# Performance work log

Measured on AMD Instinct MI355X. Metric: run time of the kernel, lower is better.

## Reference

```python
import jax, jax.numpy as jnp
import numpy as np

B, E, H, N_TAYLOR = 8192, 256, 4096, 4
BN_EPS = 1e-5


def setup_inputs() -> dict:
    key = jax.random.key(0)
    ks = jax.random.split(key, 6)
    s = 0.02
    return {
        "z1": jax.random.normal(ks[0], (B, E), jnp.float32),
        "z2": jax.random.normal(ks[1], (B, E), jnp.float32),
        "p1": jax.random.normal(ks[2], (B, E), jnp.float32),
        "p2": jax.random.normal(ks[3], (B, E), jnp.float32),
        "W1": jax.random.normal(ks[4], (E, H), jnp.float32) * s,
        "gamma": jnp.ones((H,), jnp.float32),
        "beta": jnp.zeros((H,), jnp.float32),
        "W2": jax.random.normal(ks[5], (H, E), jnp.float32) * s,
        "b2": jnp.zeros((E,), jnp.float32),
        "lamda_inv": jnp.asarray(100.0, jnp.float32),
    }


def _predictor(z, W1, gamma, beta, W2, b2):
    h = z @ W1                                   # [B, H]
    mu = jnp.mean(h, axis=0)
    var = jnp.mean(jnp.square(h - mu), axis=0)   # biased var (torch BN training)
    h = (h - mu) * jax.lax.rsqrt(var + BN_EPS) * gamma + beta
    h = jax.nn.relu(h)
    return h @ W2 + b2                           # [B, E]


def _l2norm(x):
    n = jnp.linalg.norm(x, axis=1, keepdims=True)
    return x / jnp.maximum(n, 1e-12)


def _mec(view1, view2, lamda_inv):
    v1, v2 = _l2norm(view1), _l2norm(view2)
    c = (v1 @ v2.T) / lamda_inv                  # [B, B]
    power = c
    sum_p = jnp.zeros_like(c)
    for k in range(1, N_TAYLOR + 1):
        if k > 1:
            power = power @ c
        sign = 1.0 if (k + 1) % 2 == 0 else -1.0
        sum_p = sum_p + sign * power / k
    return jnp.trace(sum_p)


def reference(z1, z2, p1, p2, W1, gamma, beta, W2, b2, lamda_inv):
    q1 = _predictor(z1, W1, gamma, beta, W2, b2)
    q2 = _predictor(z2, W1, gamma, beta, W2, b2)
    loss = (_mec(p1, q2, lamda_inv) + _mec(p2, q1, lamda_inv)) * 0.5 / B
    return -loss * lamda_inv
```

## Files before the change

### kernel.cpp

```cpp
#include <hip/hip_runtime.h>

#define B_ROWS 8192
#define E_DIM  256
#define H_DIM  4096

typedef __attribute__((ext_vector_type(8))) short short8;
typedef __attribute__((ext_vector_type(4))) float f32x4;

typedef __attribute__((address_space(1))) const void* gas1_t;
typedef __attribute__((address_space(3))) void*       las3_t;

__device__ __forceinline__ float b2f(unsigned short s) {
    return __uint_as_float(((unsigned)s) << 16);
}
__device__ __forceinline__ unsigned short f2b(float f) {
    unsigned u = __float_as_uint(f);
    u += 0x7fffu + ((u >> 16) & 1u);
    return (unsigned short)(u >> 16);
}

__device__ __forceinline__ int swz(int row, int slot) {
    return slot ^ ((row >> 1) & 3);
}

__global__ void k_transpose_cast(const float* __restrict__ in,
                                 unsigned short* __restrict__ out,
                                 int R, int C) {
    __shared__ float tile[32][33];
    const int c0 = blockIdx.x * 32, r0 = blockIdx.y * 32;
    const int tx = threadIdx.x & 31, ty = threadIdx.x >> 5;
#pragma unroll
    for (int j = 0; j < 4; ++j)
        tile[ty * 4 + j][tx] = in[(size_t)(r0 + ty * 4 + j) * C + c0 + tx];
    __syncthreads();
#pragma unroll
    for (int j = 0; j < 4; ++j)
        out[(size_t)(c0 + ty * 4 + j) * R + r0 + tx] = f2b(tile[tx][ty * 4 + j]);
}

__global__ void k_cast_bf16(const float* __restrict__ in,
                            unsigned short* __restrict__ out, int n4) {
    int i = blockIdx.x * blockDim.x + threadIdx.x;
    if (i < n4) {
        float4 v = ((const float4*)in)[i];
        ushort4 o;
        o.x = f2b(v.x); o.y = f2b(v.y); o.z = f2b(v.z); o.w = f2b(v.w);
        ((ushort4*)out)[i] = o;
    }
}

__global__ __launch_bounds__(256) void k_gemm1(
    const unsigned short* __restrict__ A, const unsigned short* __restrict__ Bt,
    unsigned short* __restrict__ Cout,
    float* __restrict__ cs, float* __restrict__ cs2,
    int M, int N, int K) {
    constexpr int BK = 32, BM = 128, BN = 128;
    constexpr int MI = 4, NI = 4;
    __shared__ __align__(16) short As[BM * BK];
    __shared__ __align__(16) short Bs[BN * BK];

    const int t = threadIdx.x;
    const int lane = t & 63, wv = t >> 6;
    const int wr = wv >> 1, wc = wv & 1;
    const int l15 = lane & 15, quad = lane >> 4;
    const int m0 = blockIdx.y * BM, n0 = blockIdx.x * BN;

    f32x4 acc[MI][NI] = {};

    for (int k0 = 0; k0 < K; k0 += BK) {
#pragma unroll
        for (int q = 0; q < 2; ++q) {
            int u = q * 256 + t;
            int row = u >> 2, kc = swz(row, u & 3);
            const short* gp = (const short*)A + (size_t)(m0 + row) * K + k0 + kc * 8;
            short* lp = As + (size_t)(q * 256 + (wv << 6)) * 8;
            __builtin_amdgcn_global_load_lds((gas1_t)gp, (las3_t)lp, 16, 0, 0);
        }
#pragma unroll
        for (int q = 0; q < 2; ++q) {
            int u = q * 256 + t;
            int row = u >> 2, kc = swz(row, u & 3);
            const short* gp = (const short*)Bt + (size_t)(n0 + row) * K + k0 + kc * 8;
            short* lp = Bs + (size_t)(q * 256 + (wv << 6)) * 8;
            __builtin_amdgcn_global_load_lds((gas1_t)gp, (las3_t)lp, 16, 0, 0);
        }
        __syncthreads();

        short8 af[MI], bfr[NI];
#pragma unroll
        for (int mi = 0; mi < MI; ++mi) {
            int row = wr * 64 + mi * 16 + l15;
            af[mi] = *(const short8*)(As + row * BK + (swz(row, quad) << 3));
        }
#pragma unroll
        for (int ni = 0; ni < NI; ++ni) {
            int row = wc * 64 + ni * 16 + l15;
            bfr[ni] = *(const short8*)(Bs + row * BK + (swz(row, quad) << 3));
        }
#pragma unroll
        for (int mi = 0; mi < MI; ++mi)
#pragma unroll
            for (int ni = 0; ni < NI; ++ni)
                acc[mi][ni] = __builtin_amdgcn_mfma_f32_16x16x32_bf16(
                    af[mi], bfr[ni], acc[mi][ni], 0, 0, 0);
        __syncthreads();
    }

#pragma unroll
    for (int ni = 0; ni < NI; ++ni) {
        float s = 0.f, s2 = 0.f;
#pragma unroll
        for (int mi = 0; mi < MI; ++mi)
#pragma unroll
            for (int r = 0; r < 4; ++r) {
                int row = m0 + wr * 64 + mi * 16 + quad * 4 + r;
                int col = n0 + wc * 64 + ni * 16 + l15;
                float v = acc[mi][ni][r];
                Cout[(size_t)row * N + col] = f2b(v);
                s += v; s2 += v * v;
            }
        s  += __shfl_xor(s, 16);  s  += __shfl_xor(s, 32);
        s2 += __shfl_xor(s2, 16); s2 += __shfl_xor(s2, 32);
        if (quad == 0) {
            int col = n0 + wc * 64 + ni * 16 + l15;
            atomicAdd(&cs[col], s);
            atomicAdd(&cs2[col], s2);
        }
    }
}

__global__ void k_bnprep(const float* __restrict__ sum, const float* __restrict__ sumsq,
                         const float* __restrict__ gamma, const float* __restrict__ beta,
                         unsigned* __restrict__ ssb) {
    int j = blockIdx.x * 256 + threadIdx.x;
    float mu = sum[j] * (1.f / B_ROWS);
    float var = sumsq[j] * (1.f / B_ROWS) - mu * mu;
    float sc = gamma[j] * rsqrtf(var + 1e-5f);
    float sh = beta[j] - mu * sc;
    ssb[j] = ((unsigned)f2b(sc) << 16) | (unsigned)f2b(sh);
}

__device__ __forceinline__ short8 bnrelu8(uint4 hv, uint4 sa, uint4 sb) {
    const unsigned short* hu = (const unsigned short*)&hv;
    const unsigned* wa = (const unsigned*)&sa;
    const unsigned* wb = (const unsigned*)&sb;
    short8 o;
#pragma unroll
    for (int j = 0; j < 8; ++j) {
        unsigned w = j < 4 ? wa[j] : wb[j - 4];
        float sc = __uint_as_float(w & 0xffff0000u);
        float sh = __uint_as_float(w << 16);
        float v = fmaxf(b2f(hu[j]) * sc + sh, 0.f);
        o[j] = (short)f2b(v);
    }
    return o;
}

__global__ __launch_bounds__(256) void k_gemm2d(
    const unsigned short* __restrict__ A, const unsigned short* __restrict__ Bt,
    float* __restrict__ Cout, const float* __restrict__ bias,
    const unsigned* __restrict__ ssb,
    int M, int N, int K) {
    constexpr int BK = 32, BM = 64, BN = 128;
    constexpr int MI = 2, NI = 4;
    __shared__ __align__(16) short As[2][BM * BK];
    __shared__ __align__(16) short Bs[2][BN * BK];

    const int t = threadIdx.x;
    const int lane = t & 63, wv = t >> 6;
    const int wr = wv >> 1, wc = wv & 1;
    const int l15 = lane & 15, quad = lane >> 4;
    const int m0 = blockIdx.y * BM, n0 = blockIdx.x * BN;

    const int Kc = K / gridDim.z;
    const int kbeg = blockIdx.z * Kc;
    const int ITERS = Kc / BK;

    const int arow = t >> 2, akc = t & 3;
    const unsigned short* hp = A + (size_t)(m0 + arow) * K + akc * 8;
    const unsigned* ssp = ssb + akc * 8;
    const int awoff = arow * BK + (swz(arow, akc) << 3);

    const unsigned short* bp0 = Bt + (size_t)(n0 + arow) * K + akc * 8;
    const unsigned short* bp1 = Bt + (size_t)(n0 + 64 + arow) * K + akc * 8;
    const int bwoff0 = arow * BK + (swz(arow, akc) << 3);
    const int bwoff1 = (64 + arow) * BK + (swz(64 + arow, akc) << 3);

    f32x4 acc[MI][NI] = {};

    uint4 hreg = *(const uint4*)(hp + kbeg);
    uint4 sa = *(const uint4*)(ssp + kbeg);
    uint4 sb = *(const uint4*)(ssp + kbeg + 4);
    uint4 b0 = *(const uint4*)(bp0 + kbeg);
    uint4 b1 = *(const uint4*)(bp1 + kbeg);

    for (int i = 0; i < ITERS; ++i) {
        const int k0 = kbeg + i * BK;
        short* Ab = As[i & 1];
        short* Bb = Bs[i & 1];

        *(short8*)(Ab + awoff) = bnrelu8(hreg, sa, sb);
        *(uint4*)(Bb + bwoff0) = b0;
        *(uint4*)(Bb + bwoff1) = b1;
        __syncthreads();

        const int kn = (i + 1 < ITERS) ? k0 + BK : kbeg;
        hreg = *(const uint4*)(hp + kn);
        sa = *(const uint4*)(ssp + kn);
        sb = *(const uint4*)(ssp + kn + 4);
        b0 = *(const uint4*)(bp0 + kn);
        b1 = *(const uint4*)(bp1 + kn);

        short8 af[MI], bfr[NI];
#pragma unroll
        for (int mi = 0; mi < MI; ++mi) {
            int row = wr * 32 + mi * 16 + l15;
            af[mi] = *(const short8*)(Ab + row * BK + (swz(row, quad) << 3));
        }
#pragma unroll
        for (int ni = 0; ni < NI; ++ni) {
            int row = wc * 64 + ni * 16 + l15;
            bfr[ni] = *(const short8*)(Bb + row * BK + (swz(row, quad) << 3));
        }
#pragma unroll
        for (int mi = 0; mi < MI; ++mi)
#pragma unroll
            for (int ni = 0; ni < NI; ++ni)
                acc[mi][ni] = __builtin_amdgcn_mfma_f32_16x16x32_bf16(
                    af[mi], bfr[ni], acc[mi][ni], 0, 0, 0);
    }

#pragma unroll
    for (int mi = 0; mi < MI; ++mi)
#pragma unroll
        for (int ni = 0; ni < NI; ++ni)
#pragma unroll
            for (int r = 0; r < 4; ++r) {
                int row = m0 + wr * 32 + mi * 16 + quad * 4 + r;
                int col = n0 + wc * 64 + ni * 16 + l15;
                float v = acc[mi][ni][r];
                if (blockIdx.z == 0) v += bias[col];
                atomicAdd(&Cout[(size_t)row * N + col], v);
            }
}

__global__ __launch_bounds__(256) void k_ntc(
    const float* __restrict__ x0, const float* __restrict__ x1,
    const float* __restrict__ x2, const float* __restrict__ x3,
    unsigned short* __restrict__ o0, unsigned short* __restrict__ o1,
    unsigned short* __restrict__ o2, unsigned short* __restrict__ o3) {
    const int z = blockIdx.y;
    const float* x = z == 0 ? x0 : z == 1 ? x1 : z == 2 ? x2 : x3;
    unsigned short* out = z == 0 ? o0 : z == 1 ? o1 : z == 2 ? o2 : o3;

    __shared__ float tile[32][264];
    __shared__ float red[32][8];
    __shared__ float invs[32];
    const int t = threadIdx.x;
    const int r0 = blockIdx.x * 32;

#pragma unroll
    for (int i = 0; i < 8; ++i) {
        int u = i * 256 + t;
        int row = u >> 6, cp = (u & 63) * 4;
        float4 v = *(const float4*)(x + (size_t)(r0 + row) * E_DIM + cp);
        *(float4*)&tile[row][cp] = v;
    }
    __syncthreads();
    {
        int row = t >> 3, cg = (t & 7) * 32;
        float s = 0.f;
#pragma unroll
        for (int j = 0; j < 32; ++j) { float v = tile[row][cg + j]; s += v * v; }
        red[row][t & 7] = s;
    }
    __syncthreads();
    if (t < 32) {
        float s = 0.f;
#pragma unroll
        for (int j = 0; j < 8; ++j) s += red[t][j];
        invs[t] = 1.f / fmaxf(sqrtf(s), 1e-12f);
    }
    __syncthreads();
    {
        int row = t & 31, cb = (t >> 5) * 32;
        float inv = invs[row];
#pragma unroll
        for (int j = 0; j < 32; ++j) {
            int c = cb + j;
            out[(size_t)c * B_ROWS + r0 + row] = f2b(tile[row][c] * inv);
        }
    }
}

#define GKS 16
__global__ __launch_bounds__(256) void k_gram(
    const unsigned short* __restrict__ p1T, const unsigned short* __restrict__ q2T,
    const unsigned short* __restrict__ p2T, const unsigned short* __restrict__ q1T,
    float* __restrict__ Ma, float* __restrict__ Mb) {
    constexpr int BK = 32;
    const int mec = blockIdx.z >> 4, kz = blockIdx.z & 15;
    const unsigned short* A = mec ? p2T : p1T;
    const unsigned short* Bt = mec ? q1T : q2T;
    float* Mout = mec ? Mb : Ma;

    __shared__ __align__(16) short As[64 * BK];
    __shared__ __align__(16) short Bs[64 * BK];

    const int t = threadIdx.x;
    const int lane = t & 63, wv = t >> 6;
    const int wr = wv >> 1, wc = wv & 1;
    const int l15 = lane & 15, quad = lane >> 4;
    const int m0 = blockIdx.y * 64, n0 = blockIdx.x * 64;
    const int kbeg = kz * (B_ROWS / GKS);

    f32x4 acc[2][2] = {};

    for (int k0 = kbeg; k0 < kbeg + B_ROWS / GKS; k0 += BK) {
        {
            int row = t >> 2, kc = swz(row, t & 3);
            const short* gpa = (const short*)A + (size_t)(m0 + row) * B_ROWS + k0 + kc * 8;
            short* lpa = As + (size_t)(wv << 6) * 8;
            __builtin_amdgcn_global_load_lds((gas1_t)gpa, (las3_t)lpa, 16, 0, 0);
            const short* gpb = (const short*)Bt + (size_t)(n0 + row) * B_ROWS + k0 + kc * 8;
            short* lpb = Bs + (size_t)(wv << 6) * 8;
            __builtin_amdgcn_global_load_lds((gas1_t)gpb, (las3_t)lpb, 16, 0, 0);
        }
        __syncthreads();

        short8 af[2], bfr[2];
#pragma unroll
        for (int mi = 0; mi < 2; ++mi) {
            int row = wr * 32 + mi * 16 + l15;
            af[mi] = *(const short8*)(As + row * BK + (swz(row, quad) << 3));
        }
#pragma unroll
        for (int ni = 0; ni < 2; ++ni) {
            int row = wc * 32 + ni * 16 + l15;
            bfr[ni] = *(const short8*)(Bs + row * BK + (swz(row, quad) << 3));
        }
#pragma unroll
        for (int mi = 0; mi < 2; ++mi)
#pragma unroll
            for (int ni = 0; ni < 2; ++ni)
                acc[mi][ni] = __builtin_amdgcn_mfma_f32_16x16x32_bf16(
                    af[mi], bfr[ni], acc[mi][ni], 0, 0, 0);
        __syncthreads();
    }

#pragma unroll
    for (int mi = 0; mi < 2; ++mi)
#pragma unroll
        for (int ni = 0; ni < 2; ++ni)
#pragma unroll
            for (int r = 0; r < 4; ++r) {
                int row = m0 + wr * 32 + mi * 16 + quad * 4 + r;
                int col = n0 + wc * 32 + ni * 16 + l15;
                atomicAdd(&Mout[(size_t)row * E_DIM + col], acc[mi][ni][r]);
            }
}

__global__ void k_m2(const float* __restrict__ Ma, const float* __restrict__ Mb,
                     float* __restrict__ M2a, float* __restrict__ M2b) {
    const float* M = blockIdx.z ? Mb : Ma;
    float* M2 = blockIdx.z ? M2b : M2a;
    int b = blockIdx.x * 16 + (threadIdx.x & 15);
    int a = blockIdx.y * 16 + (threadIdx.x >> 4);
    float s = 0.f;
    for (int k = 0; k < E_DIM; ++k) s += M[a * E_DIM + k] * M[k * E_DIM + b];
    M2[a * E_DIM + b] = s;
}

__global__ __launch_bounds__(256) void k_traces2(
    const float* __restrict__ Ma, const float* __restrict__ M2a,
    const float* __restrict__ Mb, const float* __restrict__ M2b,
    const float* __restrict__ lam, float* __restrict__ out) {
    const float* M  = blockIdx.z ? Mb  : Ma;
    const float* M2 = blockIdx.z ? M2b : M2a;
    const int i0 = blockIdx.y * 32, j0 = blockIdx.x * 32;
    const int t = threadIdx.x, col = t & 31, row = t >> 5;

    __shared__ float A[32][33], Bt[32][33], A2[32][33], B2[32][33];
#pragma unroll
    for (int r = 0; r < 4; ++r) {
        int rr = r * 8 + row;
        A [rr][col] = M [(i0 + rr) * E_DIM + j0 + col];
        Bt[rr][col] = M [(j0 + rr) * E_DIM + i0 + col];
        A2[rr][col] = M2[(i0 + rr) * E_DIM + j0 + col];
        B2[rr][col] = M2[(j0 + rr) * E_DIM + i0 + col];
    }
    __syncthreads();

    float lamv = lam[0];
    float il = 1.f / lamv;
    float F = -0.5f * lamv * (1.f / B_ROWS);
    float c1 = F * il;
    float c2 = -F * 0.5f * il * il;
    float c3 = F * (1.f / 3.f) * il * il * il;
    float c4 = -F * 0.25f * il * il * il * il;

    float s = 0.f;
#pragma unroll
    for (int r = 0; r < 4; ++r) {
        int rr = r * 8 + row;
        float mij = A[rr][col], mji = Bt[col][rr];
        float m2ij = A2[rr][col], m2ji = B2[col][rr];
        s += c2 * mij * mji + c3 * m2ij * mji + c4 * m2ij * m2ji;
        if (i0 + rr == j0 + col) s += c1 * mij;
    }
#pragma unroll
    for (int o = 32; o; o >>= 1) s += __shfl_down(s, o);
    __shared__ float red[4];
    if ((t & 63) == 0) red[t >> 6] = s;
    __syncthreads();
    if (t == 0) atomicAdd(out, red[0] + red[1] + red[2] + red[3]);
}

extern "C" void kernel_launch(void* const* d_in, const int* in_sizes, int n_in,
                              void* d_out, int out_size, void* d_ws, size_t ws_size,
                              hipStream_t stream) {
    const float* z1 = (const float*)d_in[0];
    const float* z2 = (const float*)d_in[1];
    const float* p1 = (const float*)d_in[2];
    const float* p2 = (const float*)d_in[3];
    const float* W1 = (const float*)d_in[4];
    const float* gamma = (const float*)d_in[5];
    const float* beta = (const float*)d_in[6];
    const float* W2 = (const float*)d_in[7];
    const float* b2 = (const float*)d_in[8];
    const float* lam = (const float*)d_in[9];
    float* out = (float*)d_out;
    char* ws = (char*)d_ws;

    size_t off = 0;
    auto alloc = [&](size_t bytes) { size_t o = off; off += (bytes + 255) & ~(size_t)255; return o; };
    unsigned short* W1T = (unsigned short*)(ws + alloc((size_t)E_DIM * H_DIM * 2));
    unsigned short* W2T = (unsigned short*)(ws + alloc((size_t)H_DIM * E_DIM * 2));
    unsigned short* zb  = (unsigned short*)(ws + alloc((size_t)B_ROWS * E_DIM * 2));
    unsigned short* h   = (unsigned short*)(ws + alloc((size_t)B_ROWS * H_DIM * 2));
    float* q1 = (float*)(ws + alloc((size_t)B_ROWS * E_DIM * 4));
    float* q2 = (float*)(ws + alloc((size_t)B_ROWS * E_DIM * 4));
    float* Ma  = (float*)(ws + alloc((size_t)E_DIM * E_DIM * 4));
    float* Mb  = (float*)(ws + alloc((size_t)E_DIM * E_DIM * 4));
    float* M2a = (float*)(ws + alloc((size_t)E_DIM * E_DIM * 4));
    float* M2b = (float*)(ws + alloc((size_t)E_DIM * E_DIM * 4));
    float* cs0 = (float*)(ws + alloc(H_DIM * 4));
    float* cs0q = (float*)(ws + alloc(H_DIM * 4));
    float* cs1 = (float*)(ws + alloc(H_DIM * 4));
    float* cs1q = (float*)(ws + alloc(H_DIM * 4));
    unsigned* ssb = (unsigned*)(ws + alloc(H_DIM * 4));

    const size_t TSZ = (size_t)E_DIM * B_ROWS;
    unsigned short* p1T = h;
    unsigned short* q2T = h + TSZ;
    unsigned short* p2T = h + 2 * TSZ;
    unsigned short* q1T = h + 3 * TSZ;

    hipMemsetAsync(out, 0, sizeof(float), stream);
    hipMemsetAsync(q1, 0, ((size_t)2 * B_ROWS * E_DIM + 2 * E_DIM * E_DIM) * 4, stream);
    hipMemsetAsync(cs0, 0, (size_t)4 * H_DIM * 4, stream);

    k_transpose_cast<<<dim3(H_DIM / 32, E_DIM / 32), 256, 0, stream>>>(W1, W1T, E_DIM, H_DIM);
    k_transpose_cast<<<dim3(E_DIM / 32, H_DIM / 32), 256, 0, stream>>>(W2, W2T, H_DIM, E_DIM);

    const float* zs[2] = {z1, z2};
    float* qs[2] = {q1, q2};
    float* css[2] = {cs0, cs1};
    float* cssq[2] = {cs0q, cs1q};
    for (int v = 0; v < 2; ++v) {
        k_cast_bf16<<<dim3(B_ROWS * E_DIM / 4 / 256), 256, 0, stream>>>(zs[v], zb, B_ROWS * E_DIM / 4);
        k_gemm1<<<dim3(H_DIM / 128, B_ROWS / 128), 256, 0, stream>>>(
            zb, W1T, h, css[v], cssq[v], B_ROWS, H_DIM, E_DIM);
        k_bnprep<<<dim3(H_DIM / 256), 256, 0, stream>>>(css[v], cssq[v], gamma, beta, ssb);
        k_gemm2d<<<dim3(E_DIM / 128, B_ROWS / 64, 4), 256, 0, stream>>>(
            h, W2T, qs[v], b2, ssb, B_ROWS, E_DIM, H_DIM);
    }

    k_ntc<<<dim3(B_ROWS / 32, 4), 256, 0, stream>>>(
        p1, q2, p2, q1, p1T, q2T, p2T, q1T);

    k_gram<<<dim3(4, 4, 2 * GKS), 256, 0, stream>>>(p1T, q2T, p2T, q1T, Ma, Mb);
    k_m2<<<dim3(16, 16, 2), 256, 0, stream>>>(Ma, Mb, M2a, M2b);
    k_traces2<<<dim3(8, 8, 2), 256, 0, stream>>>(Ma, M2a, Mb, M2b, lam, out);
}
```

Measured before the change: 343.4 us.

## Widen gemm2d tile to full N, raise split-K, use packed bf16 convert

The second predictor GEMM now covers the full N=256 output width in each block. Previously the A tile went through BN+ReLU twice, once per N-block; now it is loaded and transformed only once. Split-K goes from 4 to 8 to keep the grid size, and the BN/ReLU output uses v_cvt_pk_bf16_f32 instead of manual rounding. The cost is more accumulator registers (MI×NI=16 f32x4), a larger LDS B tile, and twice as many atomicAdd partial sums into the output.

```diff
diff --git a/kernel.cpp b/kernel.cpp
--- a/kernel.cpp
+++ b/kernel.cpp
@@ -17,6 +17,12 @@
     unsigned u = __float_as_uint(f);
     u += 0x7fffu + ((u >> 16) & 1u);
     return (unsigned short)(u >> 16);
+}
+
+__device__ __forceinline__ unsigned cvt_pk_bf16(float lo, float hi) {
+    unsigned r;
+    asm("v_cvt_pk_bf16_f32 %0, %1, %2" : "=v"(r) : "v"(lo), "v"(hi));
+    return r;
 }
 
 __device__ __forceinline__ int swz(int row, int slot) {
@@ -144,16 +150,18 @@
     const unsigned short* hu = (const unsigned short*)&hv;
     const unsigned* wa = (const unsigned*)&sa;
     const unsigned* wb = (const unsigned*)&sb;
-    short8 o;
+    float f[8];
 #pragma unroll
     for (int j = 0; j < 8; ++j) {
         unsigned w = j < 4 ? wa[j] : wb[j - 4];
         float sc = __uint_as_float(w & 0xffff0000u);
         float sh = __uint_as_float(w << 16);
-        float v = fmaxf(b2f(hu[j]) * sc + sh, 0.f);
-        o[j] = (short)f2b(v);
-    }
-    return o;
+        f[j] = fmaxf(b2f(hu[j]) * sc + sh, 0.f);
+    }
+    union { unsigned u[4]; short8 s; } o;
+#pragma unroll
+    for (int j = 0; j < 4; ++j) o.u[j] = cvt_pk_bf16(f[2 * j], f[2 * j + 1]);
+    return o.s;
 }
 
 __global__ __launch_bounds__(256) void k_gemm2d(
@@ -161,8 +169,8 @@
     float* __restrict__ Cout, const float* __restrict__ bias,
     const unsigned* __restrict__ ssb,
     int M, int N, int K) {
-    constexpr int BK = 32, BM = 64, BN = 128;
-    constexpr int MI = 2, NI = 4;
+    constexpr int BK = 32, BM = 64, BN = 256;
+    constexpr int MI = 2, NI = 8;
     __shared__ __align__(16) short As[2][BM * BK];
     __shared__ __align__(16) short Bs[2][BN * BK];
 
@@ -170,7 +178,7 @@
     const int lane = t & 63, wv = t >> 6;
     const int wr = wv >> 1, wc = wv & 1;
     const int l15 = lane & 15, quad = lane >> 4;
-    const int m0 = blockIdx.y * BM, n0 = blockIdx.x * BN;
+    const int m0 = blockIdx.y * BM;
 
     const int Kc = K / gridDim.z;
     const int kbeg = blockIdx.z * Kc;
@@ -181,10 +189,8 @@
     const unsigned* ssp = ssb + akc * 8;
     const int awoff = arow * BK + (swz(arow, akc) << 3);
 
-    const unsigned short* bp0 = Bt + (size_t)(n0 + arow) * K + akc * 8;
-    const unsigned short* bp1 = Bt + (size_t)(n0 + 64 + arow) * K + akc * 8;
+    const unsigned short* bp0 = Bt + (size_t)arow * K + akc * 8;
     const int bwoff0 = arow * BK + (swz(arow, akc) << 3);
-    const int bwoff1 = (64 + arow) * BK + (swz(64 + arow, akc) << 3);
 
     f32x4 acc[MI][NI] = {};
 
@@ -192,7 +198,9 @@
     uint4 sa = *(const uint4*)(ssp + kbeg);
     uint4 sb = *(const uint4*)(ssp + kbeg + 4);
     uint4 b0 = *(const uint4*)(bp0 + kbeg);
-    uint4 b1 = *(const uint4*)(bp1 + kbeg);
+    uint4 b1 = *(const uint4*)(bp0 + (size_t)64 * K + kbeg);
+    uint4 b2r = *(const uint4*)(bp0 + (size_t)128 * K + kbeg);
+    uint4 b3 = *(const uint4*)(bp0 + (size_t)192 * K + kbeg);
 
     for (int i = 0; i < ITERS; ++i) {
         const int k0 = kbeg + i * BK;
@@ -200,8 +208,10 @@
         short* Bb = Bs[i & 1];
 
         *(short8*)(Ab + awoff) = bnrelu8(hreg, sa, sb);
-        *(uint4*)(Bb + bwoff0) = b0;
-        *(uint4*)(Bb + bwoff1) = b1;
+        *(uint4*)(Bb + bwoff0)            = b0;
+        *(uint4*)(Bb + bwoff0 + 64 * BK)  = b1;
+        *(uint4*)(Bb + bwoff0 + 128 * BK) = b2r;
+        *(uint4*)(Bb + bwoff0 + 192 * BK) = b3;
         __syncthreads();
 
         const int kn = (i + 1 < ITERS) ? k0 + BK : kbeg;
@@ -209,7 +219,9 @@
         sa = *(const uint4*)(ssp + kn);
         sb = *(const uint4*)(ssp + kn + 4);
         b0 = *(const uint4*)(bp0 + kn);
-        b1 = *(const uint4*)(bp1 + kn);
+        b1 = *(const uint4*)(bp0 + (size_t)64 * K + kn);
+        b2r = *(const uint4*)(bp0 + (size_t)128 * K + kn);
+        b3 = *(const uint4*)(bp0 + (size_t)192 * K + kn);
 
         short8 af[MI], bfr[NI];
 #pragma unroll
@@ -219,7 +231,7 @@
         }
 #pragma unroll
         for (int ni = 0; ni < NI; ++ni) {
-            int row = wc * 64 + ni * 16 + l15;
+            int row = wc * 128 + ni * 16 + l15;
             bfr[ni] = *(const short8*)(Bb + row * BK + (swz(row, quad) << 3));
         }
 #pragma unroll
@@ -237,7 +249,7 @@
 #pragma unroll
             for (int r = 0; r < 4; ++r) {
                 int row = m0 + wr * 32 + mi * 16 + quad * 4 + r;
-                int col = n0 + wc * 64 + ni * 16 + l15;
+                int col = wc * 128 + ni * 16 + l15;
                 float v = acc[mi][ni][r];
                 if (blockIdx.z == 0) v += bias[col];
                 atomicAdd(&Cout[(size_t)row * N + col], v);
@@ -472,7 +484,7 @@
         k_gemm1<<<dim3(H_DIM / 128, B_ROWS / 128), 256, 0, stream>>>(
             zb, W1T, h, css[v], cssq[v], B_ROWS, H_DIM, E_DIM);
         k_bnprep<<<dim3(H_DIM / 256), 256, 0, stream>>>(css[v], cssq[v], gamma, beta, ssb);
-        k_gemm2d<<<dim3(E_DIM / 128, B_ROWS / 64, 4), 256, 0, stream>>>(
+        k_gemm2d<<<dim3(1, B_ROWS / 64, 8), 256, 0, stream>>>(
             h, W2T, qs[v], b2, ssb, B_ROWS, E_DIM, H_DIM);
     }
 
```

Measured after the change: 378.6 us. 10.3% more time.
